# Kernel tuning notes

Hardware: AMD Instinct MI355X
Metric: run time of the kernel (lower is better)

Reference implementation:

```python
import jax, jax.numpy as jnp
import numpy as np

NUM_HEADS = 16


def setup_inputs() -> dict:
    key = jax.random.key(0)
    ks = jax.random.split(key, 5)
    B, N, C = 4, 2048, 1024
    x = jax.random.normal(ks[0], (B, N, C), dtype=jnp.float32)
    mask = jax.random.randint(ks[1], (B, N), 0, 2, dtype=jnp.int32)
    W_qkv = jax.random.normal(ks[2], (C, 3 * C), dtype=jnp.float32) * (C ** -0.5)
    W_proj = jax.random.normal(ks[3], (C, C), dtype=jnp.float32) * (C ** -0.5)
    b_proj = jnp.zeros((C,), dtype=jnp.float32)
    return {"x": x, "mask": mask, "W_qkv": W_qkv, "W_proj": W_proj, "b_proj": b_proj}


def reference(x, mask, W_qkv, W_proj, b_proj):
    B, N, C = x.shape
    H = NUM_HEADS
    hd = C // H
    scale = hd ** -0.5
    # qkv projection -> [3, B, H, N, hd]
    qkv = (x @ W_qkv).reshape(B, N, 3, H, hd).transpose(2, 0, 3, 1, 4)
    q, k, v = qkv[0], qkv[1], qkv[2]
    attn = jnp.einsum('bhqd,bhkd->bhqk', q, k) * scale  # [B,H,N,N]
    add_mask = (mask[:, None, None, :] != 1).astype(jnp.float32) * -10000.0
    attn = jax.nn.softmax(attn + add_mask, axis=-1)
    out = jnp.einsum('bhqk,bhkd->bhqd', attn, v)  # [B,H,N,hd]
    out = out.transpose(0, 2, 1, 3).reshape(B, N, C)
    return out @ W_proj + b_proj
```

## Files before the change

### kernel.cpp

```cpp
#include <hip/hip_runtime.h>

typedef unsigned short u16;
typedef unsigned int u32;
typedef unsigned long long u64;
typedef __attribute__((ext_vector_type(8))) short short8;
typedef __attribute__((ext_vector_type(4))) float f32x4;

#define MLOGC (-14426.95f)

__device__ __forceinline__ u16 f2bf(float f) {
  u32 u = __builtin_bit_cast(u32, f);
  u += 0x7fffu + ((u >> 16) & 1u);
  return (u16)(u >> 16);
}
__device__ __forceinline__ u16 f2bf_fast(float f) {
  u32 u = __builtin_bit_cast(u32, f);
  return (u16)((u + 0x8000u) >> 16);
}

__device__ __forceinline__ float fexp2(float x) {
#if __has_builtin(__builtin_amdgcn_exp2f)
  return __builtin_amdgcn_exp2f(x);
#else
  return exp2f(x);
#endif
}

__device__ __forceinline__ void glds16(u16* lds, const u16* g) {
  __builtin_amdgcn_global_load_lds(
      (const __attribute__((address_space(1))) u32*)g,
      (__attribute__((address_space(3))) u32*)lds, 16, 0, 0);
}

#define MFMA(a, b, c) __builtin_amdgcn_mfma_f32_16x16x32_bf16((a), (b), (c), 0, 0, 0)


__global__ __launch_bounds__(256) void cvt_f32_bf16(const float* __restrict__ in,
                                                    u16* __restrict__ out, int n4) {
  int i = blockIdx.x * 256 + threadIdx.x;
  if (i >= n4) return;
  float4 v = ((const float4*)in)[i];
  union { u16 s[4]; u64 ll; } u;
  u.s[0] = f2bf(v.x); u.s[1] = f2bf(v.y); u.s[2] = f2bf(v.z); u.s[3] = f2bf(v.w);
  ((u64*)out)[i] = u.ll;
}

__global__ __launch_bounds__(256) void scan_mask(const int* __restrict__ mask,
                                                 int* __restrict__ s2t,
                                                 int* __restrict__ nkbuf) {
  const int b = blockIdx.x, t = threadIdx.x;
  const int lane = t & 63, w = t >> 6;
  int m8[8], c = 0;
  #pragma unroll
  for (int j = 0; j < 8; j++) {
    m8[j] = (mask[b * 2048 + t * 8 + j] == 1);
    c += m8[j];
  }
  int incl = c;
  #pragma unroll
  for (int off = 1; off < 64; off <<= 1) {
    int v = __shfl_up(incl, off);
    if (lane >= off) incl += v;
  }
  __shared__ int wtot[4];
  __shared__ int wbase[5];
  if (lane == 63) wtot[w] = incl;
  __syncthreads();
  if (t == 0) {
    int s = 0;
    for (int i = 0; i < 4; i++) { wbase[i] = s; s += wtot[i]; }
    wbase[4] = s;
  }
  __syncthreads();
  const int nk = wbase[4];
  int urun = wbase[w] + incl - c;
  #pragma unroll
  for (int j = 0; j < 8; j++) {
    int tok = t * 8 + j;
    int slot = m8[j] ? urun : nk + (tok - urun);
    s2t[b * 2048 + slot] = b * 2048 + tok;
    urun += m8[j];
  }
  if (t == 0) nkbuf[b] = nk;
}

__global__ __launch_bounds__(256) void transpose_cvt(const float* __restrict__ Wm,
                                                     u16* __restrict__ Wt, int R, int Cc) {
  __shared__ float tile[64][65];
  const int bj = blockIdx.x, bi = blockIdx.y;
  const int t = threadIdx.x;
  const int r = t >> 4, c4 = (t & 15) << 2;
  for (int rr = r; rr < 64; rr += 16) {
    float4 v = *(const float4*)&Wm[(size_t)(bi * 64 + rr) * Cc + bj * 64 + c4];
    tile[rr][c4] = v.x; tile[rr][c4 + 1] = v.y; tile[rr][c4 + 2] = v.z; tile[rr][c4 + 3] = v.w;
  }
  __syncthreads();
  for (int rr = r; rr < 64; rr += 16) {
    union { u16 s[4]; u64 ll; } u;
    u.s[0] = f2bf(tile[c4][rr]);
    u.s[1] = f2bf(tile[c4 + 1][rr]);
    u.s[2] = f2bf(tile[c4 + 2][rr]);
    u.s[3] = f2bf(tile[c4 + 3][rr]);
    *(u64*)&Wt[(size_t)(bj * 64 + rr) * R + bi * 64 + c4] = u.ll;
  }
}

__global__ __launch_bounds__(256, 2) void gemm_fused(const u16* __restrict__ xb,
                                                     const u16* __restrict__ wqkvt,
                                                     const int* __restrict__ s2t,
                                                     const int* __restrict__ nkbuf,
                                                     u16* __restrict__ qbuf,
                                                     u16* __restrict__ kc,
                                                     u16* __restrict__ vtc) {
  __shared__ u16 Asm[128 * 64];
  __shared__ u16 Bsm[128 * 64];
  const int bid = blockIdx.x;
  const int role = bid >> 9;
  const int sub = bid & 511;
  const int tid = threadIdx.x, lane = tid & 63, w = tid >> 6;
  const int quad = lane >> 4, l15 = lane & 15;
  const int wm = (w >> 1) * 64, wn = (w & 1) * 64;
  const int srow = lane >> 3;
  const int gcc = ((lane & 7) ^ srow) * 8;
  const int rx8 = (l15 & 7);

  int m0, n0;
  const u16 *Asrc, *Bsrc;
  if (role == 2) { m0 = (sub & 7) * 128; n0 = (sub >> 3) * 128; }
  else           { m0 = (sub >> 3) * 128; n0 = (sub & 7) * 128; }
  if (role == 1 && (m0 & 2047) >= nkbuf[m0 >> 11]) return;
  if (role == 2 && (n0 & 2047) >= nkbuf[n0 >> 11]) return;

  int arow[4], brow[4];
  #pragma unroll
  for (int c = 0; c < 4; ++c) {
    int rit = (w * 4 + c) * 8 + srow;
    if (role == 0)      { arow[c] = m0 + rit;            brow[c] = n0 + rit; }
    else if (role == 1) { arow[c] = s2t[m0 + rit];       brow[c] = 1024 + n0 + rit; }
    else                { arow[c] = 2048 + m0 + rit;     brow[c] = s2t[n0 + rit]; }
  }
  Asrc = (role == 2) ? wqkvt : xb;
  Bsrc = (role == 2) ? xb : wqkvt;

  f32x4 acc[4][4];
  #pragma unroll
  for (int i = 0; i < 4; i++)
    #pragma unroll
    for (int j = 0; j < 4; j++)
      #pragma unroll
      for (int r = 0; r < 4; r++) acc[i][j][r] = 0.f;

  for (int kt = 0; kt < 1024; kt += 64) {
    __syncthreads();
    #pragma unroll
    for (int c = 0; c < 4; ++c) {
      int chunk = w * 4 + c;
      glds16(&Asm[chunk * 512], &Asrc[(size_t)arow[c] * 1024 + kt + gcc]);
      glds16(&Bsm[chunk * 512], &Bsrc[(size_t)brow[c] * 1024 + kt + gcc]);
    }
    __syncthreads();
    #pragma unroll
    for (int ks = 0; ks < 2; ++ks) {
      int pc = ((ks * 4 + quad) ^ rx8) * 8;
      short8 av[4], bv[4];
      #pragma unroll
      for (int i = 0; i < 4; i++)
        av[i] = *(const short8*)&Asm[(wm + i * 16 + l15) * 64 + pc];
      #pragma unroll
      for (int j = 0; j < 4; j++)
        bv[j] = *(const short8*)&Bsm[(wn + j * 16 + l15) * 64 + pc];
      #pragma unroll
      for (int i = 0; i < 4; i++)
        #pragma unroll
        for (int j = 0; j < 4; j++)
          acc[i][j] = MFMA(av[i], bv[j], acc[i][j]);
    }
  }

  if (role == 2) {
    #pragma unroll
    for (int j = 0; j < 4; j++) {
      int col = n0 + wn + j * 16 + l15;
      int bb = col >> 11, sl = col & 2047;
      #pragma unroll
      for (int i = 0; i < 4; i++)
        #pragma unroll
        for (int r = 0; r < 4; r++) {
          int row = m0 + wm + i * 16 + quad * 4 + r;
          vtc[(size_t)(bb * 1024 + row) * 2048 + sl] = f2bf(acc[i][j][r]);
        }
    }
  } else {
    u16* dst = (role == 0) ? qbuf : kc;
    #pragma unroll
    for (int i = 0; i < 4; i++)
      #pragma unroll
      for (int j = 0; j < 4; j++) {
        int col = n0 + wn + j * 16 + l15;
        #pragma unroll
        for (int r = 0; r < 4; r++) {
          int row = m0 + wm + i * 16 + quad * 4 + r;
          dst[(size_t)row * 1024 + col] = f2bf(acc[i][j][r]);
        }
      }
  }
}

__global__ __launch_bounds__(256, 4) void attn_kernel(const u16* __restrict__ q,
                                                      const u16* __restrict__ kc,
                                                      const u16* __restrict__ vtc,
                                                      const int* __restrict__ nkbuf,
                                                      u16* __restrict__ ao) {
  __shared__ u16 Ksm[64 * 64];
  __shared__ u16 Vsm[64 * 64];
  __shared__ u16 Psm[4 * 32 * 72];
  const int qt = blockIdx.x, h = blockIdx.y, b = blockIdx.z;
  const int tid = threadIdx.x, lane = tid & 63, w = tid >> 6;
  const int quad = lane >> 4, l15 = lane & 15;
  const int q0 = qt * 128 + w * 32;
  const int srow = lane >> 3;
  const int gcc = ((lane & 7) ^ srow) * 8;
  const int rx8 = (l15 & 7);
  const float C1 = 0.18033688f;
  const int nk = nkbuf[b];
  const int ntiles = (nk + 63) >> 6;

  short8 qf[2][2];
  #pragma unroll
  for (int i = 0; i < 2; i++)
    #pragma unroll
    for (int ks = 0; ks < 2; ks++)
      qf[i][ks] = *(const short8*)&q[(size_t)(b * 2048 + q0 + i * 16 + l15) * 1024 +
                                     h * 64 + ks * 32 + quad * 8];

  f32x4 o[2][4];
  float lsum[2][4];
  #pragma unroll
  for (int i = 0; i < 2; i++)
    #pragma unroll
    for (int r = 0; r < 4; r++) {
      lsum[i][r] = 0.f;
      #pragma unroll
      for (int jd = 0; jd < 4; jd++) o[i][jd][r] = 0.f;
    }

  for (int t = 0; t < ntiles; ++t) {
    const int k0 = t * 64;
    __syncthreads();
    #pragma unroll
    for (int c = 0; c < 2; ++c) {
      int chunk = w * 2 + c;
      int r = chunk * 8 + srow;
      glds16(&Ksm[chunk * 512], &kc[(size_t)(b * 2048 + k0 + r) * 1024 + h * 64 + gcc]);
      glds16(&Vsm[chunk * 512], &vtc[(size_t)(b * 1024 + h * 64 + r) * 2048 + k0 + gcc]);
    }
    __syncthreads();

    f32x4 s[2][4];
    #pragma unroll
    for (int i = 0; i < 2; i++)
      #pragma unroll
      for (int j = 0; j < 4; j++)
        #pragma unroll
        for (int r = 0; r < 4; r++) s[i][j][r] = 0.f;
    #pragma unroll
    for (int ks = 0; ks < 2; ks++) {
      int pc = ((ks * 4 + quad) ^ rx8) * 8;
      short8 kf[4];
      #pragma unroll
      for (int j = 0; j < 4; j++)
        kf[j] = *(const short8*)&Ksm[(j * 16 + l15) * 64 + pc];
      #pragma unroll
      for (int i = 0; i < 2; i++)
        #pragma unroll
        for (int j = 0; j < 4; j++) s[i][j] = MFMA(qf[i][ks], kf[j], s[i][j]);
    }

    float mlog[4];
    #pragma unroll
    for (int j = 0; j < 4; j++)
      mlog[j] = (k0 + j * 16 + l15 < nk) ? 0.f : MLOGC;

    #pragma unroll
    for (int i = 0; i < 2; i++) {
      #pragma unroll
      for (int r = 0; r < 4; r++) {
        int prow = i * 16 + quad * 4 + r;
        float ps = 0.f;
        #pragma unroll
        for (int j = 0; j < 4; j++) {
          float p = fexp2(__builtin_fmaf(s[i][j][r], C1, mlog[j]));
          ps += p;
          Psm[w * 2304 + prow * 72 + j * 16 + l15] = f2bf_fast(p);
        }
        lsum[i][r] += ps;
      }
    }

    #pragma unroll
    for (int ks = 0; ks < 2; ks++) {
      int pcv = ((ks * 4 + quad) ^ rx8) * 8;
      int kk = ks * 32 + quad * 8;
      short8 pf[2], vf[4];
      #pragma unroll
      for (int i = 0; i < 2; i++)
        pf[i] = *(const short8*)&Psm[w * 2304 + (i * 16 + l15) * 72 + kk];
      #pragma unroll
      for (int jd = 0; jd < 4; jd++)
        vf[jd] = *(const short8*)&Vsm[(jd * 16 + l15) * 64 + pcv];
      #pragma unroll
      for (int i = 0; i < 2; i++)
        #pragma unroll
        for (int jd = 0; jd < 4; jd++) o[i][jd] = MFMA(pf[i], vf[jd], o[i][jd]);
    }
  }

  #pragma unroll
  for (int i = 0; i < 2; i++)
    #pragma unroll
    for (int r = 0; r < 4; r++) {
      float l = lsum[i][r];
      #pragma unroll
      for (int off = 8; off >= 1; off >>= 1) l += __shfl_xor(l, off);
      float inv = 1.f / l;
      size_t row = (size_t)(b * 2048 + q0 + i * 16 + quad * 4 + r);
      #pragma unroll
      for (int jd = 0; jd < 4; jd++)
        ao[row * 1024 + h * 64 + jd * 16 + l15] = f2bf(o[i][jd][r] * inv);
    }
}

#define GEMM_MAINLOOP(A_, Bt_, K_)                                                     \
  const int tid = threadIdx.x, lane = tid & 63, w = tid >> 6;                          \
  const int quad = lane >> 4, l15 = lane & 15;                                         \
  const int m0 = blockIdx.y * 128, n0 = blockIdx.x * 128;                              \
  const int wm = (w >> 1) * 64, wn = (w & 1) * 64;                                     \
  f32x4 acc[4][4];                                                                     \
  _Pragma("unroll") for (int i = 0; i < 4; i++)                                        \
    _Pragma("unroll") for (int j = 0; j < 4; j++)                                      \
      _Pragma("unroll") for (int r = 0; r < 4; r++) acc[i][j][r] = 0.f;                \
  const int srow = lane >> 3;                                                          \
  const int gcc = ((lane & 7) ^ srow) * 8;                                             \
  const int rx8 = (l15 & 7);                                                           \
  for (int kt = 0; kt < (K_); kt += 64) {                                              \
    __syncthreads();                                                                   \
    _Pragma("unroll") for (int c = 0; c < 4; ++c) {                                    \
      int chunk = w * 4 + c;                                                           \
      int row = chunk * 8 + srow;                                                      \
      glds16(&Asm[chunk * 512], &(A_)[(size_t)(m0 + row) * (K_) + kt + gcc]);          \
      glds16(&Bsm[chunk * 512], &(Bt_)[(size_t)(n0 + row) * (K_) + kt + gcc]);         \
    }                                                                                  \
    __syncthreads();                                                                   \
    _Pragma("unroll") for (int ks = 0; ks < 2; ++ks) {                                 \
      int pc = ((ks * 4 + quad) ^ rx8) * 8;                                            \
      short8 av[4], bv[4];                                                             \
      _Pragma("unroll") for (int i = 0; i < 4; i++)                                    \
        av[i] = *(const short8*)&Asm[(wm + i * 16 + l15) * 64 + pc];                   \
      _Pragma("unroll") for (int j = 0; j < 4; j++)                                    \
        bv[j] = *(const short8*)&Bsm[(wn + j * 16 + l15) * 64 + pc];                   \
      _Pragma("unroll") for (int i = 0; i < 4; i++)                                    \
        _Pragma("unroll") for (int j = 0; j < 4; j++)                                  \
          acc[i][j] = MFMA(av[i], bv[j], acc[i][j]);                                   \
    }                                                                                  \
  }

__global__ __launch_bounds__(256, 2) void gemm_proj(const u16* __restrict__ A,
                                                    const u16* __restrict__ Bt,
                                                    const float* __restrict__ bias,
                                                    float* __restrict__ out) {
  __shared__ u16 Asm[128 * 64];
  __shared__ u16 Bsm[128 * 64];
  GEMM_MAINLOOP(A, Bt, 1024)
  #pragma unroll
  for (int j = 0; j < 4; j++) {
    int col = n0 + wn + j * 16 + l15;
    float bj = bias[col];
    #pragma unroll
    for (int i = 0; i < 4; i++) {
      #pragma unroll
      for (int r = 0; r < 4; r++) {
        int row = m0 + wm + i * 16 + quad * 4 + r;
        out[(size_t)row * 1024 + col] = acc[i][j][r] + bj;
      }
    }
  }
}

extern "C" void kernel_launch(void* const* d_in, const int* in_sizes, int n_in,
                              void* d_out, int out_size, void* d_ws, size_t ws_size,
                              hipStream_t stream) {
  (void)in_sizes; (void)n_in; (void)out_size; (void)ws_size;
  const float* x     = (const float*)d_in[0];
  const int*   mask  = (const int*)d_in[1];
  const float* Wqkv  = (const float*)d_in[2];
  const float* Wproj = (const float*)d_in[3];
  const float* bproj = (const float*)d_in[4];
  float* out = (float*)d_out;
  char* ws = (char*)d_ws;

  size_t off = 0;
  u16* xb     = (u16*)(ws + off); off += 8192ull * 1024 * 2;
  u16* wqkvt  = (u16*)(ws + off); off += 3072ull * 1024 * 2;
  u16* wprojt = (u16*)(ws + off); off += 1024ull * 1024 * 2;
  u16* qbuf   = (u16*)(ws + off); off += 8192ull * 1024 * 2;
  u16* kcbuf  = (u16*)(ws + off); off += 4096ull * 2048 * 2;
  u16* vtcbuf = (u16*)(ws + off); off += 4096ull * 2048 * 2;
  u16* aobuf  = (u16*)(ws + off); off += 8192ull * 1024 * 2;
  int* s2t    = (int*)(ws + off); off += 8192ull * 4;
  int* nkbuf  = (int*)(ws + off); off += 4 * 4;

  cvt_f32_bf16<<<8192, 256, 0, stream>>>(x, xb, 2097152);
  scan_mask<<<4, 256, 0, stream>>>(mask, s2t, nkbuf);
  transpose_cvt<<<dim3(48, 16), 256, 0, stream>>>(Wqkv, wqkvt, 1024, 3072);
  transpose_cvt<<<dim3(16, 16), 256, 0, stream>>>(Wproj, wprojt, 1024, 1024);
  gemm_fused<<<1536, 256, 0, stream>>>(xb, wqkvt, s2t, nkbuf, qbuf, kcbuf, vtcbuf);
  attn_kernel<<<dim3(16, 16, 4), 256, 0, stream>>>(qbuf, kcbuf, vtcbuf, nkbuf, aobuf);
  gemm_proj<<<dim3(8, 64), 256, 0, stream>>>(aobuf, wprojt, bproj, out);
}
```

Baseline: 250.7 us.

## Merge preprocessing kernels into one launch and raise GEMM occupancy bounds

Four small preprocessing kernels (x conversion, mask scan, and two weight transpose-converts) become a single block-dispatched prep kernel, which removes three launches and the gaps between them. The launch_bounds minimum-blocks hint on both GEMM kernels goes from 2 to 3, pushing the compiler toward fewer registers for higher occupancy, with a risk of spills. The GEMM macro is inlined by hand into gemm_proj, and the bf16 rounding helper in the attention kernel is replaced by an inline equivalent. The merged kernel allocates the 64x65 float tile for every block, including the conversion blocks that never use it, which may limit occupancy for those blocks.

```diff
diff --git a/kernel.cpp b/kernel.cpp
--- a/kernel.cpp
+++ b/kernel.cpp
@@ -12,10 +12,6 @@
   u32 u = __builtin_bit_cast(u32, f);
   u += 0x7fffu + ((u >> 16) & 1u);
   return (u16)(u >> 16);
-}
-__device__ __forceinline__ u16 f2bf_fast(float f) {
-  u32 u = __builtin_bit_cast(u32, f);
-  return (u16)((u + 0x8000u) >> 16);
 }
 
 __device__ __forceinline__ float fexp2(float x) {
@@ -35,20 +31,49 @@
 #define MFMA(a, b, c) __builtin_amdgcn_mfma_f32_16x16x32_bf16((a), (b), (c), 0, 0, 0)
 
 
-__global__ __launch_bounds__(256) void cvt_f32_bf16(const float* __restrict__ in,
-                                                    u16* __restrict__ out, int n4) {
-  int i = blockIdx.x * 256 + threadIdx.x;
-  if (i >= n4) return;
-  float4 v = ((const float4*)in)[i];
-  union { u16 s[4]; u64 ll; } u;
-  u.s[0] = f2bf(v.x); u.s[1] = f2bf(v.y); u.s[2] = f2bf(v.z); u.s[3] = f2bf(v.w);
-  ((u64*)out)[i] = u.ll;
-}
-
-__global__ __launch_bounds__(256) void scan_mask(const int* __restrict__ mask,
-                                                 int* __restrict__ s2t,
-                                                 int* __restrict__ nkbuf) {
-  const int b = blockIdx.x, t = threadIdx.x;
+__global__ __launch_bounds__(256) void prep(const float* __restrict__ x,
+                                            const int* __restrict__ mask,
+                                            const float* __restrict__ Wqkv,
+                                            const float* __restrict__ Wproj,
+                                            u16* __restrict__ xb,
+                                            u16* __restrict__ wqkvt,
+                                            u16* __restrict__ wprojt,
+                                            int* __restrict__ s2t,
+                                            int* __restrict__ nkbuf) {
+  __shared__ float tile[64][65];
+  __shared__ int wtot[4];
+  __shared__ int wbase[5];
+  const int bid = blockIdx.x, t = threadIdx.x;
+
+  if (bid < 8192) {
+    int i = bid * 256 + t;
+    float4 v = ((const float4*)x)[i];
+    union { u16 s[4]; u64 ll; } u;
+    u.s[0] = f2bf(v.x); u.s[1] = f2bf(v.y); u.s[2] = f2bf(v.z); u.s[3] = f2bf(v.w);
+    ((u64*)xb)[i] = u.ll;
+    return;
+  }
+  if (bid < 9216) {
+    const float* Wm; u16* Wt; int Cc, bj, bi;
+    if (bid < 8960) { int tt = bid - 8192; Wm = Wqkv;  Wt = wqkvt;  Cc = 3072; bj = tt % 48; bi = tt / 48; }
+    else            { int tt = bid - 8960; Wm = Wproj; Wt = wprojt; Cc = 1024; bj = tt & 15; bi = tt >> 4; }
+    const int r = t >> 4, c4 = (t & 15) << 2;
+    for (int rr = r; rr < 64; rr += 16) {
+      float4 v = *(const float4*)&Wm[(size_t)(bi * 64 + rr) * Cc + bj * 64 + c4];
+      tile[rr][c4] = v.x; tile[rr][c4 + 1] = v.y; tile[rr][c4 + 2] = v.z; tile[rr][c4 + 3] = v.w;
+    }
+    __syncthreads();
+    for (int rr = r; rr < 64; rr += 16) {
+      union { u16 s[4]; u64 ll; } u;
+      u.s[0] = f2bf(tile[c4][rr]);
+      u.s[1] = f2bf(tile[c4 + 1][rr]);
+      u.s[2] = f2bf(tile[c4 + 2][rr]);
+      u.s[3] = f2bf(tile[c4 + 3][rr]);
+      *(u64*)&Wt[(size_t)(bj * 64 + rr) * 1024 + bi * 64 + c4] = u.ll;
+    }
+    return;
+  }
+  const int b = bid - 9216;
   const int lane = t & 63, w = t >> 6;
   int m8[8], c = 0;
   #pragma unroll
@@ -62,8 +87,6 @@
     int v = __shfl_up(incl, off);
     if (lane >= off) incl += v;
   }
-  __shared__ int wtot[4];
-  __shared__ int wbase[5];
   if (lane == 63) wtot[w] = incl;
   __syncthreads();
   if (t == 0) {
@@ -84,28 +107,7 @@
   if (t == 0) nkbuf[b] = nk;
 }
 
-__global__ __launch_bounds__(256) void transpose_cvt(const float* __restrict__ Wm,
-                                                     u16* __restrict__ Wt, int R, int Cc) {
-  __shared__ float tile[64][65];
-  const int bj = blockIdx.x, bi = blockIdx.y;
-  const int t = threadIdx.x;
-  const int r = t >> 4, c4 = (t & 15) << 2;
-  for (int rr = r; rr < 64; rr += 16) {
-    float4 v = *(const float4*)&Wm[(size_t)(bi * 64 + rr) * Cc + bj * 64 + c4];
-    tile[rr][c4] = v.x; tile[rr][c4 + 1] = v.y; tile[rr][c4 + 2] = v.z; tile[rr][c4 + 3] = v.w;
-  }
-  __syncthreads();
-  for (int rr = r; rr < 64; rr += 16) {
-    union { u16 s[4]; u64 ll; } u;
-    u.s[0] = f2bf(tile[c4][rr]);
-    u.s[1] = f2bf(tile[c4 + 1][rr]);
-    u.s[2] = f2bf(tile[c4 + 2][rr]);
-    u.s[3] = f2bf(tile[c4 + 3][rr]);
-    *(u64*)&Wt[(size_t)(bj * 64 + rr) * R + bi * 64 + c4] = u.ll;
-  }
-}
-
-__global__ __launch_bounds__(256, 2) void gemm_fused(const u16* __restrict__ xb,
+__global__ __launch_bounds__(256, 3) void gemm_fused(const u16* __restrict__ xb,
                                                      const u16* __restrict__ wqkvt,
                                                      const int* __restrict__ s2t,
                                                      const int* __restrict__ nkbuf,
@@ -291,7 +293,8 @@
         for (int j = 0; j < 4; j++) {
           float p = fexp2(__builtin_fmaf(s[i][j][r], C1, mlog[j]));
           ps += p;
-          Psm[w * 2304 + prow * 72 + j * 16 + l15] = f2bf_fast(p);
+          u32 pv = __builtin_bit_cast(u32, p) + 0x8000u;
+          Psm[w * 2304 + prow * 72 + j * 16 + l15] = ((const u16*)&pv)[1];
         }
         lsum[i][r] += ps;
       }
@@ -330,47 +333,55 @@
     }
 }
 
-#define GEMM_MAINLOOP(A_, Bt_, K_)                                                     \
-  const int tid = threadIdx.x, lane = tid & 63, w = tid >> 6;                          \
-  const int quad = lane >> 4, l15 = lane & 15;                                         \
-  const int m0 = blockIdx.y * 128, n0 = blockIdx.x * 128;                              \
-  const int wm = (w >> 1) * 64, wn = (w & 1) * 64;                                     \
-  f32x4 acc[4][4];                                                                     \
-  _Pragma("unroll") for (int i = 0; i < 4; i++)                                        \
-    _Pragma("unroll") for (int j = 0; j < 4; j++)                                      \
-      _Pragma("unroll") for (int r = 0; r < 4; r++) acc[i][j][r] = 0.f;                \
-  const int srow = lane >> 3;                                                          \
-  const int gcc = ((lane & 7) ^ srow) * 8;                                             \
-  const int rx8 = (l15 & 7);                                                           \
-  for (int kt = 0; kt < (K_); kt += 64) {                                              \
-    __syncthreads();                                                                   \
-    _Pragma("unroll") for (int c = 0; c < 4; ++c) {                                    \
-      int chunk = w * 4 + c;                                                           \
-      int row = chunk * 8 + srow;                                                      \
-      glds16(&Asm[chunk * 512], &(A_)[(size_t)(m0 + row) * (K_) + kt + gcc]);          \
-      glds16(&Bsm[chunk * 512], &(Bt_)[(size_t)(n0 + row) * (K_) + kt + gcc]);         \
-    }                                                                                  \
-    __syncthreads();                                                                   \
-    _Pragma("unroll") for (int ks = 0; ks < 2; ++ks) {                                 \
-      int pc = ((ks * 4 + quad) ^ rx8) * 8;                                            \
-      short8 av[4], bv[4];                                                             \
-      _Pragma("unroll") for (int i = 0; i < 4; i++)                                    \
-        av[i] = *(const short8*)&Asm[(wm + i * 16 + l15) * 64 + pc];                   \
-      _Pragma("unroll") for (int j = 0; j < 4; j++)                                    \
-        bv[j] = *(const short8*)&Bsm[(wn + j * 16 + l15) * 64 + pc];                   \
-      _Pragma("unroll") for (int i = 0; i < 4; i++)                                    \
-        _Pragma("unroll") for (int j = 0; j < 4; j++)                                  \
-          acc[i][j] = MFMA(av[i], bv[j], acc[i][j]);                                   \
-    }                                                                                  \
-  }
-
-__global__ __launch_bounds__(256, 2) void gemm_proj(const u16* __restrict__ A,
+__global__ __launch_bounds__(256, 3) void gemm_proj(const u16* __restrict__ A,
                                                     const u16* __restrict__ Bt,
                                                     const float* __restrict__ bias,
                                                     float* __restrict__ out) {
   __shared__ u16 Asm[128 * 64];
   __shared__ u16 Bsm[128 * 64];
-  GEMM_MAINLOOP(A, Bt, 1024)
+  const int tid = threadIdx.x, lane = tid & 63, w = tid >> 6;
+  const int quad = lane >> 4, l15 = lane & 15;
+  const int m0 = blockIdx.y * 128, n0 = blockIdx.x * 128;
+  const int wm = (w >> 1) * 64, wn = (w & 1) * 64;
+  const int srow = lane >> 3;
+  const int gcc = ((lane & 7) ^ srow) * 8;
+  const int rx8 = (l15 & 7);
+  f32x4 acc[4][4];
+  #pragma unroll
+  for (int i = 0; i < 4; i++)
+    #pragma unroll
+    for (int j = 0; j < 4; j++)
+      #pragma unroll
+      for (int r = 0; r < 4; r++) acc[i][j][r] = 0.f;
+
+  for (int kt = 0; kt < 1024; kt += 64) {
+    __syncthreads();
+    #pragma unroll
+    for (int c = 0; c < 4; ++c) {
+      int chunk = w * 4 + c;
+      int row = chunk * 8 + srow;
+      glds16(&Asm[chunk * 512], &A[(size_t)(m0 + row) * 1024 + kt + gcc]);
+      glds16(&Bsm[chunk * 512], &Bt[(size_t)(n0 + row) * 1024 + kt + gcc]);
+    }
+    __syncthreads();
+    #pragma unroll
+    for (int ks = 0; ks < 2; ++ks) {
+      int pc = ((ks * 4 + quad) ^ rx8) * 8;
+      short8 av[4], bv[4];
+      #pragma unroll
+      for (int i = 0; i < 4; i++)
+        av[i] = *(const short8*)&Asm[(wm + i * 16 + l15) * 64 + pc];
+      #pragma unroll
+      for (int j = 0; j < 4; j++)
+        bv[j] = *(const short8*)&Bsm[(wn + j * 16 + l15) * 64 + pc];
+      #pragma unroll
+      for (int i = 0; i < 4; i++)
+        #pragma unroll
+        for (int j = 0; j < 4; j++)
+          acc[i][j] = MFMA(av[i], bv[j], acc[i][j]);
+    }
+  }
+
   #pragma unroll
   for (int j = 0; j < 4; j++) {
     int col = n0 + wn + j * 16 + l15;
@@ -409,10 +420,7 @@
   int* s2t    = (int*)(ws + off); off += 8192ull * 4;
   int* nkbuf  = (int*)(ws + off); off += 4 * 4;
 
-  cvt_f32_bf16<<<8192, 256, 0, stream>>>(x, xb, 2097152);
-  scan_mask<<<4, 256, 0, stream>>>(mask, s2t, nkbuf);
-  transpose_cvt<<<dim3(48, 16), 256, 0, stream>>>(Wqkv, wqkvt, 1024, 3072);
-  transpose_cvt<<<dim3(16, 16), 256, 0, stream>>>(Wproj, wprojt, 1024, 1024);
+  prep<<<9220, 256, 0, stream>>>(x, mask, Wqkv, Wproj, xb, wqkvt, wprojt, s2t, nkbuf);
   gemm_fused<<<1536, 256, 0, stream>>>(xb, wqkvt, s2t, nkbuf, qbuf, kcbuf, vtcbuf);
   attn_kernel<<<dim3(16, 16, 4), 256, 0, stream>>>(qbuf, kcbuf, vtcbuf, nkbuf, aobuf);
   gemm_proj<<<dim3(8, 64), 256, 0, stream>>>(aobuf, wprojt, bproj, out);
```

Result: faster. 236.6 us (-5.6%).
